# Kernel optimization log

Measured on AMD Instinct MI355X. Metric: run time of the kernel, lower is better.

Reference implementation:

```python
import jax, jax.numpy as jnp
import numpy as np

EPS = 1e-5  # torch LayerNorm default
H = 8       # heads_num


def _ln(t, g, b):
    m = jnp.mean(t, axis=-1, keepdims=True)
    v = jnp.var(t, axis=-1, keepdims=True)
    return (t - m) / jnp.sqrt(v + EPS) * g + b


def setup_inputs() -> dict:
    key = jax.random.key(0)
    ks = jax.random.split(key, 12)
    B, S, Dq, Dk, Dff = 4, 2048, 512, 768, 2048
    def w(k, shape, scale=0.02):
        return jax.random.normal(k, shape, jnp.float32) * scale
    return {
        "x": jax.random.normal(ks[0], (B, S, Dq), jnp.float32),
        "y": jax.random.normal(ks[1], (B, S, Dk), jnp.float32),
        # cross-attention projections (stored [in, out]; linear_q/k/v have no bias)
        "Wq": w(ks[2], (Dq, Dq)), "Wk": w(ks[3], (Dk, Dq)), "Wv": w(ks[4], (Dk, Dq)),
        "Wo": w(ks[5], (Dq, Dq)), "bo": jnp.zeros((Dq,), jnp.float32),
        # nn.MultiheadAttention packed in-projection and out-projection
        "mha_w_in": w(ks[6], (Dq, 3 * Dq)), "mha_b_in": jnp.zeros((3 * Dq,), jnp.float32),
        "mha_wo": w(ks[7], (Dq, Dq)), "mha_bo": jnp.zeros((Dq,), jnp.float32),
        # 4 LayerNorms
        "ln1_g": jnp.ones((Dq,), jnp.float32), "ln1_b": jnp.zeros((Dq,), jnp.float32),
        "ln2_g": jnp.ones((Dk,), jnp.float32), "ln2_b": jnp.zeros((Dk,), jnp.float32),
        "ln3_g": jnp.ones((Dq,), jnp.float32), "ln3_b": jnp.zeros((Dq,), jnp.float32),
        "ln4_g": jnp.ones((Dq,), jnp.float32), "ln4_b": jnp.zeros((Dq,), jnp.float32),
        # dense MLP (moe=False branch)
        "mlp_w1": w(ks[8], (Dq, Dff)), "mlp_b1": jnp.zeros((Dff,), jnp.float32),
        "mlp_w2": w(ks[9], (Dff, Dq)), "mlp_b2": jnp.zeros((Dq,), jnp.float32),
    }


def reference(x, y, Wq, Wk, Wv, Wo, bo, mha_w_in, mha_b_in, mha_wo, mha_bo,
              ln1_g, ln1_b, ln2_g, ln2_b, ln3_g, ln3_b, ln4_g, ln4_b,
              mlp_w1, mlp_b1, mlp_w2, mlp_b2):
    B, S, D = x.shape
    hd = D // H
    inv_sqrt_hd = 1.0 / np.sqrt(hd).astype(np.float32)

    xn = _ln(x, ln1_g, ln1_b)
    yn = _ln(y, ln2_g, ln2_b)

    # ---- Multi_CrossAttention: manual QK^T softmax V over true seq axis ----
    q = (xn @ Wq).reshape(B, S, H, hd)
    k = (yn @ Wk).reshape(B, -1, H, hd)
    v = (yn @ Wv).reshape(B, -1, H, hd)
    scores = jnp.einsum('bqhd,bkhd->bhqk', q, k) * inv_sqrt_hd  # [B,H,S,S] (512 MB)
    attn = jax.nn.softmax(scores, axis=-1)
    ctx = jnp.einsum('bhqk,bkhd->bqhd', attn, v).reshape(B, S, D)
    ca = ctx @ Wo + bo

    h = _ln(ca + xn, ln3_g, ln3_b)

    # ---- nn.MultiheadAttention (batch_first=False!): axis 0 is the sequence ----
    qkv = h @ mha_w_in + mha_b_in  # [L=B, N=S, 3D]
    q2, k2, v2 = jnp.split(qkv, 3, axis=-1)
    L, N = q2.shape[0], q2.shape[1]
    q2 = q2.reshape(L, N, H, hd)
    k2 = k2.reshape(L, N, H, hd)
    v2 = v2.reshape(L, N, H, hd)
    s2 = jnp.einsum('lnhd,mnhd->nhlm', q2, k2) * inv_sqrt_hd  # [N,H,L,L]
    a2 = jax.nn.softmax(s2, axis=-1)
    sa = jnp.einsum('nhlm,mnhd->lnhd', a2, v2).reshape(L, N, D) @ mha_wo + mha_bo

    h2 = _ln(sa + h, ln4_g, ln4_b)

    # ---- dense MLP (GELU exact, dropout=0) ----
    mlp = jax.nn.gelu(h2 @ mlp_w1 + mlp_b1, approximate=False) @ mlp_w2 + mlp_b2
    return mlp + h2
```

## Files before the change

### kernel.cpp

```cpp
#include <hip/hip_runtime.h>
#include <math.h>

typedef unsigned short u16;
typedef __attribute__((ext_vector_type(8))) short bf8;
typedef __attribute__((ext_vector_type(4))) float f4;
typedef __attribute__((ext_vector_type(16))) float f32x16;
typedef __attribute__((ext_vector_type(4))) unsigned int u32x4;
typedef __attribute__((ext_vector_type(2))) unsigned int u32x2;
typedef __attribute__((ext_vector_type(4))) unsigned short u16x4;
typedef __attribute__((ext_vector_type(8))) unsigned short u16x8;

__device__ __forceinline__ float bf2f(u16 a){
  unsigned u = ((unsigned)a) << 16;
  float f; __builtin_memcpy(&f, &u, 4);
  return f;
}
__device__ __forceinline__ u16 f2bf(float f){
  unsigned u; __builtin_memcpy(&u, &f, 4);
  u += 0x7fffu + ((u >> 16) & 1u);
  return (u16)(u >> 16);
}
__device__ __forceinline__ unsigned cvtpk(float a, float b){
  unsigned r;
  asm("v_cvt_pk_bf16_f32 %0, %1, %2" : "=v"(r) : "v"(a), "v"(b));
  return r;
}
__device__ __forceinline__ void plswap(unsigned &a, unsigned &b){
  asm("v_permlane32_swap_b32 %0, %1" : "+v"(a), "+v"(b));
}
__device__ __forceinline__ void gload16(const u16* g, u16* l){
  __builtin_amdgcn_global_load_lds((const __attribute__((address_space(1))) void*)g,
                                   (__attribute__((address_space(3))) void*)l, 16, 0, 0);
}
__device__ __forceinline__ int xcd_swizzle(int orig, int nwg){
  const int qq = nwg >> 3, rr = nwg & 7;
  const int xcd = orig & 7, loc = orig >> 3;
  return (xcd < rr ? xcd * (qq + 1) : rr * (qq + 1) + (xcd - rr) * qq) + loc;
}
__device__ __forceinline__ float gelu_f(float v){
  const float vc = fminf(v, 10.f);
  const float z  = vc * (1.f + 0.044715f * vc * vc);
  const float e  = __builtin_amdgcn_exp2f(2.302208499f * z);
  return v * e * __builtin_amdgcn_rcpf(e + 1.f);
}

__global__ void k_transpose_all(
    const float* __restrict__ Wq, const float* __restrict__ Wk,
    const float* __restrict__ Wv, const float* __restrict__ Wo,
    const float* __restrict__ Win, const float* __restrict__ Wmo,
    const float* __restrict__ W1, const float* __restrict__ W2,
    u16* __restrict__ WqT, u16* __restrict__ WkT, u16* __restrict__ WvT,
    u16* __restrict__ WoT, u16* __restrict__ WinT, u16* __restrict__ WmoT,
    u16* __restrict__ W1T, u16* __restrict__ W2T)
{
  __shared__ float tile[32][33];
  const int tid = blockIdx.x;
  const float* in; u16* out; int R, C, lo;
  if (tid < 1280){
    if (tid < 256)       { in = Wq;  out = WqT;  R = 512; C = 512;  lo = 0; }
    else if (tid < 640)  { in = Wk;  out = WkT;  R = 768; C = 512;  lo = 256; }
    else if (tid < 1024) { in = Wv;  out = WvT;  R = 768; C = 512;  lo = 640; }
    else                 { in = Wo;  out = WoT;  R = 512; C = 512;  lo = 1024; }
  } else {
    if (tid < 2048)      { in = Win; out = WinT; R = 512; C = 1536; lo = 1280; }
    else if (tid < 2304) { in = Wmo; out = WmoT; R = 512; C = 512;  lo = 2048; }
    else if (tid < 3328) { in = W1;  out = W1T;  R = 512; C = 2048; lo = 2304; }
    else                 { in = W2;  out = W2T;  R = 2048; C = 512; lo = 3328; }
  }
  const int local = tid - lo;
  const int tpx = C >> 5;
  const int bx = (local % tpx) * 32, by = (local / tpx) * 32;
  const int tx = threadIdx.x, ty = threadIdx.y;
#pragma unroll
  for (int i = 0; i < 4; i++)
    tile[ty + i*8][tx] = in[(size_t)(by + ty + i*8) * C + bx + tx];
  __syncthreads();
#pragma unroll
  for (int i = 0; i < 4; i++)
    out[(size_t)(bx + ty + i*8) * R + by + tx] = f2bf(tile[tx][ty + i*8]);
}

__device__ __forceinline__ void ln_row_f32(
    const float* __restrict__ r, const float* __restrict__ gam,
    const float* __restrict__ bet, u16* __restrict__ outb, int D, int t)
{
  const int nv = D >> 8;
  float v[3] = {0.f, 0.f, 0.f};
  float s = 0.f, s2 = 0.f;
#pragma unroll
  for (int i = 0; i < 3; i++){
    if (i < nv){ float xx = r[t + i*256]; v[i] = xx; s += xx; s2 += xx*xx; }
  }
#pragma unroll
  for (int m = 32; m; m >>= 1){ s += __shfl_xor(s, m); s2 += __shfl_xor(s2, m); }
  __shared__ float rs[4], rq[4];
  const int wave = t >> 6;
  if ((t & 63) == 0){ rs[wave] = s; rq[wave] = s2; }
  __syncthreads();
  s  = rs[0] + rs[1] + rs[2] + rs[3];
  s2 = rq[0] + rq[1] + rq[2] + rq[3];
  const float mean = s / (float)D;
  const float var  = s2 / (float)D - mean * mean;
  const float rstd = rsqrtf(var + 1e-5f);
#pragma unroll
  for (int i = 0; i < 3; i++){
    if (i < nv){
      const int c = t + i*256;
      outb[c] = f2bf((v[i] - mean) * rstd * gam[c] + bet[c]);
    }
  }
}

__global__ __launch_bounds__(256) void k_layernorm12(
    const float* __restrict__ x, const float* __restrict__ y,
    const float* __restrict__ g1, const float* __restrict__ b1,
    const float* __restrict__ g2, const float* __restrict__ b2,
    u16* __restrict__ xnB, u16* __restrict__ ynB)
{
  const int row = blockIdx.x;
  if (row < 8192){
    ln_row_f32(x + (size_t)row * 512, g1, b1, xnB + (size_t)row * 512, 512, threadIdx.x);
  } else {
    const int r2 = row - 8192;
    ln_row_f32(y + (size_t)r2 * 768, g2, b2, ynB + (size_t)r2 * 768, 768, threadIdx.x);
  }
}

__global__ __launch_bounds__(256) void k_layernorm_b(
    const u16* __restrict__ in, const float* __restrict__ gam,
    const float* __restrict__ bet, u16* __restrict__ outb)
{
  const int row = blockIdx.x, t = threadIdx.x;
  const u16* r = in + (size_t)row * 512;
  const float v0 = bf2f(r[t]);
  const float v1 = bf2f(r[t + 256]);
  float s = v0 + v1, s2 = v0*v0 + v1*v1;
#pragma unroll
  for (int m = 32; m; m >>= 1){ s += __shfl_xor(s, m); s2 += __shfl_xor(s2, m); }
  __shared__ float rs[4], rq[4];
  const int wave = t >> 6;
  if ((t & 63) == 0){ rs[wave] = s; rq[wave] = s2; }
  __syncthreads();
  s  = rs[0] + rs[1] + rs[2] + rs[3];
  s2 = rq[0] + rq[1] + rq[2] + rq[3];
  const float mean = s * (1.f / 512.f);
  const float var  = s2 * (1.f / 512.f) - mean * mean;
  const float rstd = rsqrtf(var + 1e-5f);
  u16* o = outb + (size_t)row * 512;
  o[t]       = f2bf((v0 - mean) * rstd * gam[t] + bet[t]);
  o[t + 256] = f2bf((v1 - mean) * rstd * gam[t + 256] + bet[t + 256]);
}

template<int TM, int TN, bool BIAS, bool RES, bool GELU_ACT, int OUTM, bool QSC = false>
__global__ __launch_bounds__(256, 4) void k_gemm(
    const u16* __restrict__ A, const u16* __restrict__ BT,
    const float* __restrict__ bias, const u16* __restrict__ res,
    float* __restrict__ outf, u16* __restrict__ outb, u16* __restrict__ outb2,
    int M, int N, int K)
{
  constexpr int MF = TM / 32;
  constexpr int NF = TN / 32;
  constexpr int WM = TM / 2;
  constexpr int WN = TN / 2;
  __shared__ u16 Sb[(TM + TN) * 64];
  const int t = threadIdx.x;
  const int gx = gridDim.x;
  const int swz = xcd_swizzle(blockIdx.y * gx + blockIdx.x, gx * gridDim.y);
  const int m0 = (swz / gx) * TM, n0 = (swz % gx) * TN;
  const int wave = t >> 6, lane = t & 63;
  const int wm = wave >> 1, wn = wave & 1;
  const int l15 = lane & 15, lg = lane >> 4;
  const u16* Ag = A + (size_t)m0 * K;
  const u16* Bg = BT + (size_t)n0 * K;

  const int lrow = lane >> 3;
  const int csrc = (((lane & 7) ^ lrow) << 3);
  const u16* Agl = Ag + (size_t)lrow * K + csrc;
  const u16* Bgl = Bg + (size_t)lrow * K + csrc;

  f4 acc[MF][NF];
#pragma unroll
  for (int i = 0; i < MF; i++)
#pragma unroll
    for (int j = 0; j < NF; j++) acc[i][j] = (f4){0.f, 0.f, 0.f, 0.f};

  const int nK = K >> 6;
#pragma unroll
  for (int i = 0; i < TM/32; i++){
    const int rb = (i*4 + wave) * 8;
    gload16(Agl + (size_t)rb * K, &Sb[rb * 64]);
  }
#pragma unroll
  for (int i = 0; i < TN/32; i++){
    const int rb = (i*4 + wave) * 8;
    gload16(Bgl + (size_t)rb * K, &Sb[(TM + rb) * 64]);
  }
  asm volatile("s_waitcnt vmcnt(0)" ::: "memory");
  __syncthreads();

  for (int kt = 0;; kt++){
    const char* As = (const char*)&Sb[0];
    const char* Bs = (const char*)&Sb[TM * 64];
#pragma unroll
    for (int kc = 0; kc < 2; kc++){
      bf8 af[MF], bfr[NF];
      const int kb = kc*64 + lg*16;
#pragma unroll
      for (int mf = 0; mf < MF; mf++){
        const int row = wm*WM + mf*16 + l15;
        af[mf] = *(const bf8*)(As + row*128 + (kb ^ ((row & 7) << 4)));
      }
#pragma unroll
      for (int nf = 0; nf < NF; nf++){
        const int row = wn*WN + nf*16 + l15;
        bfr[nf] = *(const bf8*)(Bs + row*128 + (kb ^ ((row & 7) << 4)));
      }
#pragma unroll
      for (int mf = 0; mf < MF; mf++)
#pragma unroll
        for (int nf = 0; nf < NF; nf++)
          acc[mf][nf] = __builtin_amdgcn_mfma_f32_16x16x32_bf16(af[mf], bfr[nf], acc[mf][nf], 0, 0, 0);
    }
    if (kt + 1 == nK) break;
    __syncthreads();
    const int ko = (kt + 1) << 6;
#pragma unroll
    for (int i = 0; i < TM/32; i++){
      const int rb = (i*4 + wave) * 8;
      gload16(Agl + (size_t)rb * K + ko, &Sb[rb * 64]);
    }
#pragma unroll
    for (int i = 0; i < TN/32; i++){
      const int rb = (i*4 + wave) * 8;
      gload16(Bgl + (size_t)rb * K + ko, &Sb[(TM + rb) * 64]);
    }
    asm volatile("s_waitcnt vmcnt(0)" ::: "memory");
    __syncthreads();
  }
#pragma unroll
  for (int mf = 0; mf < MF; mf++){
#pragma unroll
    for (int nf = 0; nf < NF; nf++){
      const int colg = n0 + wn*WN + nf*16 + l15;
      const int rowg = m0 + wm*WM + mf*16 + lg*4;
      const float bv = BIAS ? bias[colg] : 0.f;
      float vv[4];
#pragma unroll
      for (int j = 0; j < 4; j++){
        float v = acc[mf][nf][j] + bv;
        if (RES) v += bf2f(res[(size_t)(rowg + j) * N + colg]);
        if (GELU_ACT) v = gelu_f(v);
        if (QSC) v *= 0.1803368801f;
        vv[j] = v;
      }
      if (OUTM == 0){
#pragma unroll
        for (int j = 0; j < 4; j++) outf[(size_t)(rowg + j) * N + colg] = vv[j];
      } else if (OUTM == 1){
#pragma unroll
        for (int j = 0; j < 4; j++) outb[(size_t)(rowg + j) * N + colg] = f2bf(vv[j]);
      } else if (OUTM == 2){
        const int bb = rowg >> 11, ss = rowg & 2047;
        u16x4 pk;
#pragma unroll
        for (int j = 0; j < 4; j++) pk[j] = f2bf(vv[j]);
        *(u16x4*)(outb + ((size_t)(bb*512 + colg)) * 2048 + ss) = pk;
      } else {
        if (n0 < 512){
#pragma unroll
          for (int j = 0; j < 4; j++) outb[(size_t)(rowg + j) * 512 + colg] = f2bf(vv[j]);
        } else {
          const int bb = rowg >> 11, ss = rowg & 2047;
          u16x4 pk;
#pragma unroll
          for (int j = 0; j < 4; j++) pk[j] = f2bf(vv[j]);
          *(u16x4*)(outb2 + ((size_t)(bb*512 + (colg - 512))) * 2048 + ss) = pk;
        }
      }
    }
  }
}

__global__ __launch_bounds__(256, 2) void k_flash(
    const u16* __restrict__ q, const u16* __restrict__ k,
    const u16* __restrict__ vt, u16* __restrict__ ctx)
{
  __shared__ u16 Kb[2][128 * 64];
  __shared__ u16 Vb[2][64 * 128];
  const int t = threadIdx.x;
  const int wave = t >> 6, lane = t & 63;
  const int l31 = lane & 31, hi = lane >> 5;
  const int id = blockIdx.y * 16 + blockIdx.x;
  const int swz = xcd_swizzle(id, 512);
  const int qb = swz & 15, bh = swz >> 4;
  const int b = bh >> 3, h = bh & 7;
  const int qrow0 = qb*128 + wave*32;

  bf8 qf[4];
  {
    const u16* qp = q + ((size_t)(b*2048 + qrow0 + l31)) * 512 + h*64 + hi*8;
    qf[0] = *(const bf8*)qp;
    qf[1] = *(const bf8*)(qp + 16);
    qf[2] = *(const bf8*)(qp + 32);
    qf[3] = *(const bf8*)(qp + 48);
  }

  const int lrow8 = lane >> 3;
  const int csK = (((lane & 7) ^ lrow8) << 3);
  const u16* kgl = k + ((size_t)(b*2048 + lrow8)) * 512 + h*64 + csK;
  const int lrow4 = lane >> 4;
  const int csVe = (((lane & 15) ^ lrow4) << 3);
  const int csVo = (((lane & 15) ^ (4 + lrow4)) << 3);
  const u16* vrow = vt + ((size_t)(b*512 + h*64 + lrow4)) * 2048;

  f32x16 o0, o1;
#pragma unroll
  for (int r = 0; r < 16; r++){ o0[r] = 0.f; o1[r] = 0.f; }
  float rl = 0.f;

#pragma unroll
  for (int i = 0; i < 4; i++){
    const int rb = (i*4 + wave) * 8;
    gload16(kgl + (size_t)rb * 512, &Kb[0][rb * 64]);
    const int sl = i*4 + wave;
    gload16(vrow + (size_t)(sl*4) * 2048 + ((sl & 1) ? csVo : csVe), &Vb[0][sl * 512]);
  }

  int cur = 0;
  for (int it = 0; it < 16; it++){
    asm volatile("s_waitcnt vmcnt(0)" ::: "memory");
    __syncthreads();
    if (it + 1 < 16){
      const int kt = (it + 1) << 7;
#pragma unroll
      for (int i = 0; i < 4; i++){
        const int rb = (i*4 + wave) * 8;
        gload16(kgl + (size_t)(kt + rb) * 512, &Kb[cur^1][rb * 64]);
        const int sl = i*4 + wave;
        gload16(vrow + (size_t)(sl*4) * 2048 + kt + ((sl & 1) ? csVo : csVe),
                &Vb[cur^1][sl * 512]);
      }
    }
    const char* kbuf = (const char*)Kb[cur];
    const char* vbuf = (const char*)Vb[cur];
    f32x16 s0, s1, s2, s3;
#pragma unroll
    for (int r = 0; r < 16; r++){ s0[r] = 0.f; s1[r] = 0.f; s2[r] = 0.f; s3[r] = 0.f; }
    __builtin_amdgcn_s_setprio(1);
#pragma unroll
    for (int ds = 0; ds < 4; ds++){
      const int off = ds*32 + hi*16;
      const int r0 = l31, r1 = 32 + l31, r2 = 64 + l31, r3 = 96 + l31;
      const bf8 k0 = *(const bf8*)(kbuf + r0*128 + (off ^ ((r0 & 7) << 4)));
      const bf8 k1 = *(const bf8*)(kbuf + r1*128 + (off ^ ((r1 & 7) << 4)));
      const bf8 k2 = *(const bf8*)(kbuf + r2*128 + (off ^ ((r2 & 7) << 4)));
      const bf8 k3 = *(const bf8*)(kbuf + r3*128 + (off ^ ((r3 & 7) << 4)));
      s0 = __builtin_amdgcn_mfma_f32_32x32x16_bf16(k0, qf[ds], s0, 0, 0, 0);
      s1 = __builtin_amdgcn_mfma_f32_32x32x16_bf16(k1, qf[ds], s1, 0, 0, 0);
      s2 = __builtin_amdgcn_mfma_f32_32x32x16_bf16(k2, qf[ds], s2, 0, 0, 0);
      s3 = __builtin_amdgcn_mfma_f32_32x32x16_bf16(k3, qf[ds], s3, 0, 0, 0);
    }
    __builtin_amdgcn_s_setprio(0);
    bf8 pa[4][2];
    float rsum = 0.f;
#define SMPACK(SV, SUB)                                                        \
    {                                                                          \
      float pp[16];                                                            \
      _Pragma("unroll")                                                        \
      for (int r = 0; r < 16; r++) pp[r] = __builtin_amdgcn_exp2f(SV[r]);      \
      _Pragma("unroll")                                                        \
      for (int r = 0; r < 16; r++) rsum += pp[r];                              \
      unsigned w0 = cvtpk(pp[0],  pp[1]),  w1 = cvtpk(pp[2],  pp[3]);          \
      unsigned w2 = cvtpk(pp[4],  pp[5]),  w3 = cvtpk(pp[6],  pp[7]);          \
      unsigned w4 = cvtpk(pp[8],  pp[9]),  w5 = cvtpk(pp[10], pp[11]);         \
      unsigned w6 = cvtpk(pp[12], pp[13]), w7 = cvtpk(pp[14], pp[15]);         \
      plswap(w0, w2); plswap(w1, w3);                                          \
      plswap(w4, w6); plswap(w5, w7);                                          \
      u32x4 t0 = {w0, w1, w2, w3};                                             \
      u32x4 t1 = {w4, w5, w6, w7};                                             \
      __builtin_memcpy(&pa[SUB][0], &t0, 16);                                  \
      __builtin_memcpy(&pa[SUB][1], &t1, 16);                                  \
    }
    SMPACK(s0, 0)
    SMPACK(s1, 1)
    SMPACK(s2, 2)
    SMPACK(s3, 3)
#undef SMPACK
    rsum += __shfl_xor(rsum, 32);
    rl += rsum;
    __builtin_amdgcn_s_setprio(1);
#pragma unroll
    for (int sub = 0; sub < 4; sub++)
#pragma unroll
      for (int kt2 = 0; kt2 < 2; kt2++){
        const int off = sub*64 + kt2*32 + hi*16;
        const int r0 = l31, r1 = 32 + l31;
        const bf8 vf0 = *(const bf8*)(vbuf + r0*256 + (off ^ ((r0 & 7) << 4)));
        const bf8 vf1 = *(const bf8*)(vbuf + r1*256 + (off ^ ((r1 & 7) << 4)));
        o0 = __builtin_amdgcn_mfma_f32_32x32x16_bf16(pa[sub][kt2], vf0, o0, 0, 0, 0);
        o1 = __builtin_amdgcn_mfma_f32_32x32x16_bf16(pa[sub][kt2], vf1, o1, 0, 0, 0);
      }
    __builtin_amdgcn_s_setprio(0);
    cur ^= 1;
  }
  const float linv = 1.f / rl;
#pragma unroll
  for (int r = 0; r < 16; r++){
    const int crow = (r & 3) + 8*(r >> 2) + 4*hi;
    const float iv = __shfl(linv, crow);
    u16* cp = ctx + ((size_t)(b*2048 + qrow0 + crow)) * 512 + h*64 + l31;
    cp[0]  = f2bf(o0[r] * iv);
    cp[32] = f2bf(o1[r] * iv);
  }
}

__global__ __launch_bounds__(256) void k_mha_small(const u16* __restrict__ qkv,
                                                   u16* __restrict__ outb)
{
  const int tid = blockIdx.x * 256 + threadIdx.x;
  const int n = tid & 2047;
  const int hl = tid >> 11;
  const int h = hl >> 2, l = hl & 3;
  const u16* qp = qkv + ((size_t)l * 2048 + n) * 1536 + h*64;
  float qv[64];
#pragma unroll
  for (int i = 0; i < 8; i++){
    const bf8 c = *(const bf8*)(qp + i*8);
#pragma unroll
    for (int j2 = 0; j2 < 8; j2++) qv[i*8 + j2] = bf2f((u16)c[j2]) * 0.125f;
  }
  float sc[4];
#pragma unroll
  for (int m = 0; m < 4; m++){
    const u16* kp = qkv + ((size_t)m * 2048 + n) * 1536 + 512 + h*64;
    float a = 0.f;
#pragma unroll
    for (int i = 0; i < 8; i++){
      const bf8 c = *(const bf8*)(kp + i*8);
#pragma unroll
      for (int j2 = 0; j2 < 8; j2++) a += qv[i*8 + j2] * bf2f((u16)c[j2]);
    }
    sc[m] = a;
  }
  const float mx = fmaxf(fmaxf(sc[0], sc[1]), fmaxf(sc[2], sc[3]));
  float p[4]; float sum = 0.f;
#pragma unroll
  for (int m = 0; m < 4; m++){ p[m] = __expf(sc[m] - mx); sum += p[m]; }
  const float inv = 1.f / sum;
  float ov[64];
#pragma unroll
  for (int i = 0; i < 64; i++) ov[i] = 0.f;
#pragma unroll
  for (int m = 0; m < 4; m++){
    const float pw = p[m] * inv;
    const u16* vp = qkv + ((size_t)m * 2048 + n) * 1536 + 1024 + h*64;
#pragma unroll
    for (int i = 0; i < 8; i++){
      const bf8 c = *(const bf8*)(vp + i*8);
#pragma unroll
      for (int j2 = 0; j2 < 8; j2++) ov[i*8 + j2] += pw * bf2f((u16)c[j2]);
    }
  }
  u16* op = outb + ((size_t)l * 2048 + n) * 512 + h*64;
#pragma unroll
  for (int i = 0; i < 8; i++){
    u16x8 pk;
#pragma unroll
    for (int j2 = 0; j2 < 8; j2++) pk[j2] = f2bf(ov[i*8 + j2]);
    *(u16x8*)(op + i*8) = pk;
  }
}

extern "C" void kernel_launch(void* const* d_in, const int* in_sizes, int n_in,
                              void* d_out, int out_size, void* d_ws, size_t ws_size,
                              hipStream_t stream)
{
  (void)in_sizes; (void)n_in; (void)out_size; (void)ws_size;
  const float* x    = (const float*)d_in[0];
  const float* y    = (const float*)d_in[1];
  const float* Wq   = (const float*)d_in[2];
  const float* Wk   = (const float*)d_in[3];
  const float* Wv   = (const float*)d_in[4];
  const float* Wo   = (const float*)d_in[5];
  const float* bo   = (const float*)d_in[6];
  const float* Win  = (const float*)d_in[7];
  const float* bin  = (const float*)d_in[8];
  const float* Wmo  = (const float*)d_in[9];
  const float* bmo  = (const float*)d_in[10];
  const float* ln1g = (const float*)d_in[11];
  const float* ln1b = (const float*)d_in[12];
  const float* ln2g = (const float*)d_in[13];
  const float* ln2b = (const float*)d_in[14];
  const float* ln3g = (const float*)d_in[15];
  const float* ln3b = (const float*)d_in[16];
  const float* ln4g = (const float*)d_in[17];
  const float* ln4b = (const float*)d_in[18];
  const float* W1   = (const float*)d_in[19];
  const float* b1   = (const float*)d_in[20];
  const float* W2   = (const float*)d_in[21];
  const float* b2   = (const float*)d_in[22];

  char* ws = (char*)d_ws;
  const size_t MB = 1024 * 1024;
  u16* WqT  = (u16*)ws;
  u16* WkT  = WqT  + 512 * 512;
  u16* WvT  = WkT  + 512 * 768;
  u16* WoT  = WvT  + 512 * 768;
  u16* WinT = WoT  + 512 * 512;
  u16* WmoT = WinT + 1536 * 512;
  u16* W1T  = WmoT + 512 * 512;
  u16* W2T  = W1T  + 2048 * 512;
  u16* xnB  = (u16*)(ws +   9 * MB);
  u16* ynB  = (u16*)(ws +  17 * MB);
  u16* qB   = (u16*)(ws +  29 * MB);
  u16* kB   = (u16*)(ws +  37 * MB);
  u16* vtB  = (u16*)(ws +  45 * MB);
  u16* ctxB = (u16*)(ws +  53 * MB);
  u16* carB = (u16*)(ws +  61 * MB);
  u16* hB   = (u16*)(ws +  69 * MB);
  u16* qkvB = (u16*)(ws +  77 * MB);
  u16* saB  = (u16*)(ws + 101 * MB);
  u16* sarB = qB;
  u16* h2B  = kB;
  u16* t1B  = vtB;

  k_transpose_all<<<4352, dim3(32, 8), 0, stream>>>(
      Wq, Wk, Wv, Wo, Win, Wmo, W1, W2,
      WqT, WkT, WvT, WoT, WinT, WmoT, W1T, W2T);

  k_layernorm12<<<16384, 256, 0, stream>>>(x, y, ln1g, ln1b, ln2g, ln2b, xnB, ynB);

  k_gemm<64,128,false,false,false,1,true><<<dim3(4, 128), 256, 0, stream>>>(xnB, WqT, nullptr, nullptr, nullptr, qB, nullptr, 8192, 512, 512);
  k_gemm<64,128,false,false,false,3><<<dim3(8, 128), 256, 0, stream>>>(ynB, WkT, nullptr, nullptr, nullptr, kB, vtB,   8192, 1024, 768);

  k_flash<<<dim3(16, 32), 256, 0, stream>>>(qB, kB, vtB, ctxB);

  k_gemm<64,128,true,true,false,1><<<dim3(4, 128), 256, 0, stream>>>(ctxB, WoT, bo, xnB, nullptr, carB, nullptr, 8192, 512, 512);
  k_layernorm_b<<<8192, 256, 0, stream>>>(carB, ln3g, ln3b, hB);

  k_gemm<128,128,true,false,false,1><<<dim3(12, 64), 256, 0, stream>>>(hB, WinT, bin, nullptr, nullptr, qkvB, nullptr, 8192, 1536, 512);
  k_mha_small<<<256, 256, 0, stream>>>(qkvB, saB);
  k_gemm<64,128,true,true,false,1><<<dim3(4, 128), 256, 0, stream>>>(saB, WmoT, bmo, hB, nullptr, sarB, nullptr, 8192, 512, 512);
  k_layernorm_b<<<8192, 256, 0, stream>>>(sarB, ln4g, ln4b, h2B);

  k_gemm<128,128,true,false,true,1><<<dim3(16, 64), 256, 0, stream>>>(h2B, W1T, b1, nullptr, nullptr, t1B, nullptr, 8192, 2048, 512);
  k_gemm<64,128,true,true,false,0><<<dim3(4, 128), 256, 0, stream>>>(t1B, W2T, b2, h2B, (float*)d_out, nullptr, nullptr, 8192, 512, 2048);
}
```

Before: 214.1 us.

## Single-buffer K tile and interleave softmax with PV MFMAs in flash kernel

```diff
diff --git a/kernel.cpp b/kernel.cpp
--- a/kernel.cpp
+++ b/kernel.cpp
@@ -281,11 +281,11 @@
   }
 }
 
-__global__ __launch_bounds__(256, 2) void k_flash(
+__global__ __launch_bounds__(256, 3) void k_flash(
     const u16* __restrict__ q, const u16* __restrict__ k,
     const u16* __restrict__ vt, u16* __restrict__ ctx)
 {
-  __shared__ u16 Kb[2][128 * 64];
+  __shared__ u16 Kb[128 * 64];
   __shared__ u16 Vb[2][64 * 128];
   const int t = threadIdx.x;
   const int wave = t >> 6, lane = t & 63;
@@ -321,7 +321,7 @@
 #pragma unroll
   for (int i = 0; i < 4; i++){
     const int rb = (i*4 + wave) * 8;
-    gload16(kgl + (size_t)rb * 512, &Kb[0][rb * 64]);
+    gload16(kgl + (size_t)rb * 512, &Kb[rb * 64]);
     const int sl = i*4 + wave;
     gload16(vrow + (size_t)(sl*4) * 2048 + ((sl & 1) ? csVo : csVe), &Vb[0][sl * 512]);
   }
@@ -334,14 +334,12 @@
       const int kt = (it + 1) << 7;
 #pragma unroll
       for (int i = 0; i < 4; i++){
-        const int rb = (i*4 + wave) * 8;
-        gload16(kgl + (size_t)(kt + rb) * 512, &Kb[cur^1][rb * 64]);
         const int sl = i*4 + wave;
         gload16(vrow + (size_t)(sl*4) * 2048 + kt + ((sl & 1) ? csVo : csVe),
                 &Vb[cur^1][sl * 512]);
       }
     }
-    const char* kbuf = (const char*)Kb[cur];
+    const char* kbuf = (const char*)Kb;
     const char* vbuf = (const char*)Vb[cur];
     f32x16 s0, s1, s2, s3;
 #pragma unroll
@@ -361,9 +359,17 @@
       s3 = __builtin_amdgcn_mfma_f32_32x32x16_bf16(k3, qf[ds], s3, 0, 0, 0);
     }
     __builtin_amdgcn_s_setprio(0);
-    bf8 pa[4][2];
+    __syncthreads();
+    if (it + 1 < 16){
+      const int kt = (it + 1) << 7;
+#pragma unroll
+      for (int i = 0; i < 4; i++){
+        const int rb = (i*4 + wave) * 8;
+        gload16(kgl + (size_t)(kt + rb) * 512, &Kb[rb * 64]);
+      }
+    }
     float rsum = 0.f;
-#define SMPACK(SV, SUB)                                                        \
+#define SMPV(SV, SUB)                                                          \
     {                                                                          \
       float pp[16];                                                            \
       _Pragma("unroll")                                                        \
@@ -378,29 +384,28 @@
       plswap(w4, w6); plswap(w5, w7);                                          \
       u32x4 t0 = {w0, w1, w2, w3};                                             \
       u32x4 t1 = {w4, w5, w6, w7};                                             \
-      __builtin_memcpy(&pa[SUB][0], &t0, 16);                                  \
-      __builtin_memcpy(&pa[SUB][1], &t1, 16);                                  \
-    }
-    SMPACK(s0, 0)
-    SMPACK(s1, 1)
-    SMPACK(s2, 2)
-    SMPACK(s3, 3)
-#undef SMPACK
+      bf8 pa0, pa1;                                                            \
+      __builtin_memcpy(&pa0, &t0, 16);                                         \
+      __builtin_memcpy(&pa1, &t1, 16);                                         \
+      const int off0 = SUB*64 + hi*16;                                         \
+      const int off1 = SUB*64 + 32 + hi*16;                                    \
+      const int r0 = l31, r1 = 32 + l31;                                       \
+      const bf8 va0 = *(const bf8*)(vbuf + r0*256 + (off0 ^ ((r0 & 7) << 4))); \
+      const bf8 va1 = *(const bf8*)(vbuf + r1*256 + (off0 ^ ((r1 & 7) << 4))); \
+      const bf8 vb0 = *(const bf8*)(vbuf + r0*256 + (off1 ^ ((r0 & 7) << 4))); \
+      const bf8 vb1 = *(const bf8*)(vbuf + r1*256 + (off1 ^ ((r1 & 7) << 4))); \
+      o0 = __builtin_amdgcn_mfma_f32_32x32x16_bf16(pa0, va0, o0, 0, 0, 0);     \
+      o1 = __builtin_amdgcn_mfma_f32_32x32x16_bf16(pa0, va1, o1, 0, 0, 0);     \
+      o0 = __builtin_amdgcn_mfma_f32_32x32x16_bf16(pa1, vb0, o0, 0, 0, 0);     \
+      o1 = __builtin_amdgcn_mfma_f32_32x32x16_bf16(pa1, vb1, o1, 0, 0, 0);     \
+    }
+    SMPV(s0, 0)
+    SMPV(s1, 1)
+    SMPV(s2, 2)
+    SMPV(s3, 3)
+#undef SMPV
     rsum += __shfl_xor(rsum, 32);
     rl += rsum;
-    __builtin_amdgcn_s_setprio(1);
-#pragma unroll
-    for (int sub = 0; sub < 4; sub++)
-#pragma unroll
-      for (int kt2 = 0; kt2 < 2; kt2++){
-        const int off = sub*64 + kt2*32 + hi*16;
-        const int r0 = l31, r1 = 32 + l31;
-        const bf8 vf0 = *(const bf8*)(vbuf + r0*256 + (off ^ ((r0 & 7) << 4)));
-        const bf8 vf1 = *(const bf8*)(vbuf + r1*256 + (off ^ ((r1 & 7) << 4)));
-        o0 = __builtin_amdgcn_mfma_f32_32x32x16_bf16(pa[sub][kt2], vf0, o0, 0, 0, 0);
-        o1 = __builtin_amdgcn_mfma_f32_32x32x16_bf16(pa[sub][kt2], vf1, o1, 0, 0, 0);
-      }
-    __builtin_amdgcn_s_setprio(0);
     cur ^= 1;
   }
   const float linv = 1.f / rl;
```

Result: no change. 212.0 us, median of 2 (-1.0%).
